# Performance work log

Hardware: AMD Instinct MI355X
Metric: run time of the kernel (lower is better)

## Reference

```python
import jax, jax.numpy as jnp
import numpy as np

C = 256

def setup_inputs() -> dict:
    key = jax.random.key(0)
    k1, k2, k3, k4, k5 = jax.random.split(key, 5)
    x = jax.random.normal(k1, (4, C, 64, 64), dtype=jnp.float32)
    # conv1x1 weights stored as (out, in) matrices
    w_qkv = jax.random.normal(k2, (3 * C, C), dtype=jnp.float32) * (1.0 / np.sqrt(C))
    b_qkv = jax.random.normal(k3, (3 * C,), dtype=jnp.float32) * 0.01
    w_out = jax.random.normal(k4, (C, C), dtype=jnp.float32) * (1.0 / np.sqrt(C))
    b_out = jax.random.normal(k5, (C,), dtype=jnp.float32) * 0.01
    return {"x": x, "w_qkv": w_qkv, "b_qkv": b_qkv, "w_out": w_out, "b_out": b_out}

def reference(x, w_qkv, b_qkv, w_out, b_out):
    b, c, h, w = x.shape
    # norm = Identity. conv1x1 == channel matmul
    qkv = jnp.einsum('bchw,oc->bohw', x, w_qkv) + b_qkv[None, :, None, None]
    q, k, v = jnp.split(qkv, 3, axis=1)  # each (b, c, h, w)
    q = q.reshape(b, c, h * w).transpose(0, 2, 1)  # (b, hw, c)
    k = k.reshape(b, c, h * w)                      # (b, c, hw)
    v = v.reshape(b, c, h * w).transpose(0, 2, 1)  # (b, hw, c)
    scores = jnp.einsum('bnc,bcm->bnm', q, k) * (c ** -0.5)  # (b, hw, hw)
    attn = jax.nn.softmax(scores, axis=-1)
    out = jnp.einsum('bnm,bmc->bnc', attn, v)  # (b, hw, c)
    out = out.transpose(0, 2, 1).reshape(b, c, h, w)
    out = jnp.einsum('bchw,oc->bohw', out, w_out) + b_out[None, :, None, None]
    return out + x
```

## Files before the change

kernel.cpp:

```cpp
#include <hip/hip_runtime.h>
#include <hip/hip_bf16.h>
#include <hip/hip_fp16.h>
#include <math.h>

typedef short s16x8 __attribute__((ext_vector_type(8)));
typedef float f32x4 __attribute__((ext_vector_type(4)));
typedef float f32x16 __attribute__((ext_vector_type(16)));
typedef unsigned short u16x4 __attribute__((ext_vector_type(4)));
typedef unsigned int u32x4 __attribute__((ext_vector_type(4)));

#define CCH 256
#define SEQ 4096
#define NB 4
#define KVB 64

static __device__ __forceinline__ unsigned short f2bf(float f) {
  union { float f; unsigned int u; } v; v.f = f;
  unsigned int u = v.u;
  unsigned int r = u + 0x7FFFu + ((u >> 16) & 1u);
  return (unsigned short)(r >> 16);
}

static __device__ __forceinline__ void gl16(const void* g, void* l) {
  __builtin_amdgcn_global_load_lds(
      (const __attribute__((address_space(1))) void*)g,
      (__attribute__((address_space(3))) void*)l, 16, 0, 0);
}

static __device__ __forceinline__ unsigned int cvt_pk_bf16(float lo, float hi) {
  unsigned int w;
  asm("v_cvt_pk_bf16_f32 %0, %1, %2" : "=v"(w) : "v"(lo), "v"(hi));
  return w;
}

__global__ __launch_bounds__(256) void prep(
    const float* __restrict__ wqkv, const float* __restrict__ wout,
    unsigned short* __restrict__ wqkb, unsigned short* __restrict__ wob)
{
  int bid = blockIdx.x;
  int tid = threadIdx.x;
  const float* src; unsigned short* dst; int i;
  if (bid < 192) { src = wqkv; dst = wqkb; i = bid * 256 + tid; }
  else           { src = wout; dst = wob;  i = (bid - 192) * 256 + tid; }
  float4 v = ((const float4*)src)[i];
  u16x4 r;
  r.x = f2bf(v.x); r.y = f2bf(v.y); r.z = f2bf(v.z); r.w = f2bf(v.w);
  ((u16x4*)dst)[i] = r;
}

__global__ __launch_bounds__(512) void qkv_proj(
    const float* __restrict__ x, const unsigned short* __restrict__ wqkb,
    const float* __restrict__ bias,
    unsigned short* __restrict__ qb, unsigned short* __restrict__ kb,
    unsigned short* __restrict__ vb)
{
  __shared__ __align__(16) unsigned short T[32][256];
  int b = blockIdx.y, st = blockIdx.x;
  int tid = threadIdx.x, w = tid >> 6, l = tid & 63, l15 = l & 15, lg = l >> 4;
  int sbase = st * 32;
  int s7 = l15 & 7;

  #pragma unroll
  for (int i = 0; i < 4; i++) {
    int idx = i * 512 + tid;
    int sc = idx & 7, ch = idx >> 3;
    float4 v = *(const float4*)&x[((size_t)b * CCH + ch) * SEQ + sbase + sc * 4];
    #pragma unroll
    for (int j = 0; j < 4; j++) {
      int s = sc * 4 + j;
      int csw = (((ch >> 3) ^ (s & 7)) << 3) | (ch & 7);
      float fv = (j == 0) ? v.x : (j == 1) ? v.y : (j == 2) ? v.z : v.w;
      T[s][csw] = f2bf(fv);
    }
  }
  __syncthreads();

  if (w < 4) {
    int sloc = (w & 1) * 16;
    int row0 = sbase + sloc;
    int osel = w >> 1;
    s16x8 af[8];
    #pragma unroll
    for (int t = 0; t < 8; t++)
      af[t] = *(const s16x8*)&T[sloc + l15][(((t * 4 + lg) ^ s7)) * 8];

    unsigned short* dst = osel ? kb : qb;
    #pragma unroll
    for (int ot = 0; ot < 16; ot++) {
      int orow = osel * 256 + ot * 16;
      f32x4 acc = (f32x4){0.f, 0.f, 0.f, 0.f};
      #pragma unroll
      for (int t = 0; t < 8; t++) {
        s16x8 wf = *(const s16x8*)&wqkb[(size_t)(orow + l15) * CCH + t * 32 + lg * 8];
        acc = __builtin_amdgcn_mfma_f32_16x16x32_bf16(af[t], wf, acc, 0, 0, 0);
      }
      float bi = bias[orow + l15];
      int ch = ot * 16 + l15;
      #pragma unroll
      for (int r = 0; r < 4; r++) {
        int srow = row0 + lg * 4 + r;
        dst[((size_t)b * SEQ + srow) * CCH + ch] = f2bf(acc[r] + bi);
      }
    }
  } else {
    int obase = (w - 4) * 64;
    f32x4 acc[4][2];
    #pragma unroll
    for (int i = 0; i < 4; i++)
      #pragma unroll
      for (int j = 0; j < 2; j++) acc[i][j] = (f32x4){0.f, 0.f, 0.f, 0.f};

    #pragma unroll
    for (int kt = 0; kt < 8; kt++) {
      s16x8 afr[4], bfr[2];
      #pragma unroll
      for (int ot = 0; ot < 4; ot++)
        afr[ot] = *(const s16x8*)&wqkb[(size_t)(512 + obase + ot * 16 + l15) * CCH + kt * 32 + lg * 8];
      #pragma unroll
      for (int sj = 0; sj < 2; sj++)
        bfr[sj] = *(const s16x8*)&T[sj * 16 + l15][(((kt * 4 + lg) ^ s7)) * 8];
      #pragma unroll
      for (int ot = 0; ot < 4; ot++)
        #pragma unroll
        for (int sj = 0; sj < 2; sj++)
          acc[ot][sj] = __builtin_amdgcn_mfma_f32_16x16x32_bf16(afr[ot], bfr[sj], acc[ot][sj], 0, 0, 0);
    }

    #pragma unroll
    for (int ot = 0; ot < 4; ot++) {
      #pragma unroll
      for (int r = 0; r < 4; r++) {
        int o = obase + ot * 16 + lg * 4 + r;
        float bi = bias[512 + o];
        #pragma unroll
        for (int sj = 0; sj < 2; sj++) {
          int s = sbase + sj * 16 + l15;
          vb[((size_t)b * CCH + o) * SEQ + s] = f2bf(acc[ot][sj][r] + bi);
        }
      }
    }
  }
}

template<int NSPLIT_>
__global__ __launch_bounds__(512, 2) void attn_kernel(
    const unsigned short* __restrict__ qb,
    const unsigned short* __restrict__ kb,
    const unsigned short* __restrict__ vb,
    __half* __restrict__ pacc, float* __restrict__ llp)
{
  constexpr int KVLEN_ = SEQ / NSPLIT_;
  constexpr int NT_ = KVLEN_ / KVB;
  __shared__ __align__(16) unsigned short Ks[2][KVB * CCH];
  __shared__ __align__(16) unsigned short Vs[2][CCH * KVB];

  int b = blockIdx.z, kvh = blockIdx.y, qt = blockIdx.x;
  int tid = threadIdx.x, w = tid >> 6, l = tid & 63;
  int l31 = l & 31, lh = l >> 5;
  int s7 = l31 & 7;

  int qrow0 = qt * 256 + w * 32;
  const unsigned short* qptr = qb + ((size_t)b * SEQ + qrow0 + l31) * CCH + lh * 8;
  s16x8 qf[16];
  #pragma unroll
  for (int t = 0; t < 16; t++) qf[t] = *(const s16x8*)(qptr + t * 16);

  f32x16 oacc[8];
  #pragma unroll
  for (int i = 0; i < 8; i++)
    #pragma unroll
    for (int j = 0; j < 16; j++) oacc[i][j] = 0.f;
  float ll = 0.f;

  int koff0 = (tid >> 5) * CCH + (((tid & 31) ^ ((tid >> 5) & 7)) * 8);
  int voff0 = (tid >> 3) * SEQ + (((tid & 7) ^ ((tid >> 3) & 7)) * 8);
  const unsigned short* kbb = kb + (size_t)b * SEQ * CCH + (size_t)kvh * KVLEN_ * CCH;
  const unsigned short* vbb = vb + (size_t)b * CCH * SEQ + kvh * KVLEN_;

  auto stage = [&](int bf_, int kv) {
    #pragma unroll
    for (int i = 0; i < 4; i++)
      gl16(kbb + (size_t)kv * KVB * CCH + koff0 + i * 16 * CCH, &Ks[bf_][(i * 512 + tid) * 8]);
    #pragma unroll
    for (int i = 0; i < 4; i++)
      gl16(vbb + kv * KVB + voff0 + (size_t)i * 64 * SEQ, &Vs[bf_][(i * 512 + tid) * 8]);
  };

  stage(0, 0);
  __syncthreads();

  int buf = 0;
  for (int kv = 0; kv < NT_; kv++) {
    if (kv + 1 < NT_) stage(buf ^ 1, kv + 1);

    #pragma unroll
    for (int h = 0; h < 2; h++) {
      f32x16 sacc;
      #pragma unroll
      for (int i = 0; i < 16; i++) sacc[i] = 0.f;
      __builtin_amdgcn_s_setprio(1);
      #pragma unroll
      for (int st = 0; st < 16; st++) {
        s16x8 kf = *(const s16x8*)&Ks[buf][(h * 32 + l31) * CCH + (((st * 2 + lh) ^ s7) * 8)];
        sacc = __builtin_amdgcn_mfma_f32_32x32x16_bf16(kf, qf[st], sacc, 0, 0, 0);
      }
      __builtin_amdgcn_s_setprio(0);

      unsigned int pw[8];
      #pragma unroll
      for (int r = 0; r < 8; r++) {
        float p0 = __builtin_amdgcn_exp2f(fmaf(sacc[2 * r],     0.09016844f, -11.5415602f));
        float p1 = __builtin_amdgcn_exp2f(fmaf(sacc[2 * r + 1], 0.09016844f, -11.5415602f));
        ll += p0 + p1;
        pw[r] = cvt_pk_bf16(p0, p1);
      }
      asm volatile("v_permlane32_swap_b32 %0, %1" : "+v"(pw[0]), "+v"(pw[2]));
      asm volatile("v_permlane32_swap_b32 %0, %1" : "+v"(pw[1]), "+v"(pw[3]));
      asm volatile("v_permlane32_swap_b32 %0, %1" : "+v"(pw[4]), "+v"(pw[6]));
      asm volatile("v_permlane32_swap_b32 %0, %1" : "+v"(pw[5]), "+v"(pw[7]));
      u32x4 pa0u = {pw[0], pw[1], pw[2], pw[3]};
      u32x4 pa1u = {pw[4], pw[5], pw[6], pw[7]};
      s16x8 pa0 = *(s16x8*)&pa0u;
      s16x8 pa1 = *(s16x8*)&pa1u;

      __builtin_amdgcn_s_setprio(1);
      #pragma unroll
      for (int dt = 0; dt < 8; dt++) {
        int base = (dt * 32 + l31) * KVB;
        s16x8 vf0 = *(const s16x8*)&Vs[buf][base + (((h * 4 + lh) ^ s7) * 8)];
        oacc[dt] = __builtin_amdgcn_mfma_f32_32x32x16_bf16(pa0, vf0, oacc[dt], 0, 0, 0);
        s16x8 vf1 = *(const s16x8*)&Vs[buf][base + (((h * 4 + 2 + lh) ^ s7) * 8)];
        oacc[dt] = __builtin_amdgcn_mfma_f32_32x32x16_bf16(pa1, vf1, oacc[dt], 0, 0, 0);
      }
      __builtin_amdgcn_s_setprio(0);
    }

    __syncthreads();
    buf ^= 1;
  }

  ll += __shfl_xor(ll, 32);
  size_t pbase = (size_t)(b * NSPLIT_ + kvh) * SEQ;
  if (lh == 0) llp[pbase + qrow0 + l31] = ll;
  __half* pb_ = pacc + (pbase + qrow0) * CCH + l31;
  #pragma unroll
  for (int rg = 0; rg < 4; rg++)
    #pragma unroll
    for (int j = 0; j < 4; j++) {
      int qr = j + 8 * rg + 4 * lh;
      #pragma unroll
      for (int dt = 0; dt < 8; dt++)
        pb_[(size_t)qr * CCH + dt * 32] = __float2half(oacc[dt][rg * 4 + j]);
    }
}

template<int NS>
__global__ __launch_bounds__(256) void out_proj(
    const __half* __restrict__ pacc, const float* __restrict__ llp,
    const unsigned short* __restrict__ wb,
    const float* __restrict__ bias, const float* __restrict__ x,
    float* __restrict__ out)
{
  int b = blockIdx.y, st = blockIdx.x;
  int tid = threadIdx.x, w = tid >> 6, l = tid & 63, l15 = l & 15, lg = l >> 4;
  int sbase = st * 32, obase = w * 64;

  float inv[2];
  #pragma unroll
  for (int sj = 0; sj < 2; sj++) {
    int s = sbase + sj * 16 + l15;
    float den = 0.f;
    #pragma unroll
    for (int k = 0; k < NS; k++) den += llp[(size_t)(b * NS + k) * SEQ + s];
    inv[sj] = 1.f / den;
  }

  f32x4 acc[4][2];
  #pragma unroll
  for (int i = 0; i < 4; i++)
    #pragma unroll
    for (int j = 0; j < 2; j++) acc[i][j] = (f32x4){0.f, 0.f, 0.f, 0.f};

  #pragma unroll
  for (int kt = 0; kt < 8; kt++) {
    s16x8 af[4], bfr[2];
    #pragma unroll
    for (int ot = 0; ot < 4; ot++)
      af[ot] = *(const s16x8*)&wb[(obase + ot * 16 + l15) * CCH + kt * 32 + lg * 8];
    #pragma unroll
    for (int sj = 0; sj < 2; sj++) {
      int s = sbase + sj * 16 + l15;
      float facc[8] = {0.f, 0.f, 0.f, 0.f, 0.f, 0.f, 0.f, 0.f};
      #pragma unroll
      for (int k = 0; k < NS; k++) {
        const __half* p = pacc + ((size_t)(b * NS + k) * SEQ + s) * CCH + kt * 32 + lg * 8;
        u16x4 h0 = *(const u16x4*)(p);
        u16x4 h1 = *(const u16x4*)(p + 4);
        #pragma unroll
        for (int j = 0; j < 4; j++) {
          facc[j]     += __half2float(*(const __half*)&((const unsigned short*)&h0)[j]);
          facc[4 + j] += __half2float(*(const __half*)&((const unsigned short*)&h1)[j]);
        }
      }
      unsigned short tmp[8];
      #pragma unroll
      for (int j = 0; j < 4; j++) {
        tmp[j]     = f2bf(facc[j] * inv[sj]);
        tmp[4 + j] = f2bf(facc[4 + j] * inv[sj]);
      }
      bfr[sj] = *(s16x8*)tmp;
    }
    #pragma unroll
    for (int ot = 0; ot < 4; ot++)
      #pragma unroll
      for (int sj = 0; sj < 2; sj++)
        acc[ot][sj] = __builtin_amdgcn_mfma_f32_16x16x32_bf16(af[ot], bfr[sj], acc[ot][sj], 0, 0, 0);
  }

  #pragma unroll
  for (int ot = 0; ot < 4; ot++) {
    #pragma unroll
    for (int r = 0; r < 4; r++) {
      int o = obase + ot * 16 + lg * 4 + r;
      float bi = bias[o];
      #pragma unroll
      for (int sj = 0; sj < 2; sj++) {
        int s = sbase + sj * 16 + l15;
        size_t idx = ((size_t)b * CCH + o) * SEQ + s;
        out[idx] = acc[ot][sj][r] + bi + x[idx];
      }
    }
  }
}

extern "C" void kernel_launch(void* const* d_in, const int* in_sizes, int n_in,
                              void* d_out, int out_size, void* d_ws, size_t ws_size,
                              hipStream_t stream) {
  const float* x     = (const float*)d_in[0];
  const float* w_qkv = (const float*)d_in[1];
  const float* b_qkv = (const float*)d_in[2];
  const float* w_out = (const float*)d_in[3];
  const float* b_out = (const float*)d_in[4];
  float* out = (float*)d_out;

  char* ws = (char*)d_ws;
  unsigned short* qbp  = (unsigned short*)(ws);
  unsigned short* kbp  = (unsigned short*)(ws + ((size_t)8 << 20));
  unsigned short* vbp  = (unsigned short*)(ws + ((size_t)16 << 20));
  unsigned short* wqkb = (unsigned short*)(ws + ((size_t)24 << 20));
  unsigned short* wob  = (unsigned short*)(ws + ((size_t)24 << 20) + (512u << 10));
  float*          llp  = (float*)(ws + ((size_t)25 << 20));
  __half*         pacc = (__half*)(ws + ((size_t)26 << 20));

  prep<<<dim3(256), 256, 0, stream>>>(w_qkv, w_out, wqkb, wob);
  qkv_proj<<<dim3(128, NB), 512, 0, stream>>>(x, wqkb, b_qkv, qbp, kbp, vbp);

  bool split4 = ws_size >= ((size_t)60 << 20);
  if (split4) {
    attn_kernel<4><<<dim3(16, 4, NB), 512, 0, stream>>>(qbp, kbp, vbp, pacc, llp);
    out_proj<4><<<dim3(128, NB), 256, 0, stream>>>(pacc, llp, wob, b_out, x, out);
  } else {
    attn_kernel<2><<<dim3(16, 2, NB), 512, 0, stream>>>(qbp, kbp, vbp, pacc, llp);
    out_proj<2><<<dim3(128, NB), 256, 0, stream>>>(pacc, llp, wob, b_out, x, out);
  }
}
```

Before: 150.0 us.

## Interleave second-half QK^T MFMAs with first-half PV MFMAs in attention loop

Restructures the per-KV-tile loop so the QK^T MFMAs for the second 32-row half are issued interleaved with the PV MFMAs of the first half. The goal is to overlap the softmax exp/permute latency with matrix work instead of running score, exp and PV strictly in sequence. The output-projection kernel also merges two 8-byte fp16 loads into one 16-byte load. It moves the 1/l normalization out of the per-element bf16 conversion into the final epilogue, which slightly changes rounding since unnormalized sums are converted to bf16.

```diff
diff --git a/kernel.cpp b/kernel.cpp
--- a/kernel.cpp
+++ b/kernel.cpp
@@ -7,6 +7,7 @@
 typedef float f32x4 __attribute__((ext_vector_type(4)));
 typedef float f32x16 __attribute__((ext_vector_type(16)));
 typedef unsigned short u16x4 __attribute__((ext_vector_type(4)));
+typedef unsigned short u16x8 __attribute__((ext_vector_type(8)));
 typedef unsigned int u32x4 __attribute__((ext_vector_type(4)));
 
 #define CCH 256
@@ -193,47 +194,82 @@
   for (int kv = 0; kv < NT_; kv++) {
     if (kv + 1 < NT_) stage(buf ^ 1, kv + 1);
 
-    #pragma unroll
-    for (int h = 0; h < 2; h++) {
-      f32x16 sacc;
-      #pragma unroll
-      for (int i = 0; i < 16; i++) sacc[i] = 0.f;
-      __builtin_amdgcn_s_setprio(1);
-      #pragma unroll
-      for (int st = 0; st < 16; st++) {
-        s16x8 kf = *(const s16x8*)&Ks[buf][(h * 32 + l31) * CCH + (((st * 2 + lh) ^ s7) * 8)];
-        sacc = __builtin_amdgcn_mfma_f32_32x32x16_bf16(kf, qf[st], sacc, 0, 0, 0);
-      }
-      __builtin_amdgcn_s_setprio(0);
-
-      unsigned int pw[8];
-      #pragma unroll
-      for (int r = 0; r < 8; r++) {
-        float p0 = __builtin_amdgcn_exp2f(fmaf(sacc[2 * r],     0.09016844f, -11.5415602f));
-        float p1 = __builtin_amdgcn_exp2f(fmaf(sacc[2 * r + 1], 0.09016844f, -11.5415602f));
-        ll += p0 + p1;
-        pw[r] = cvt_pk_bf16(p0, p1);
-      }
-      asm volatile("v_permlane32_swap_b32 %0, %1" : "+v"(pw[0]), "+v"(pw[2]));
-      asm volatile("v_permlane32_swap_b32 %0, %1" : "+v"(pw[1]), "+v"(pw[3]));
-      asm volatile("v_permlane32_swap_b32 %0, %1" : "+v"(pw[4]), "+v"(pw[6]));
-      asm volatile("v_permlane32_swap_b32 %0, %1" : "+v"(pw[5]), "+v"(pw[7]));
-      u32x4 pa0u = {pw[0], pw[1], pw[2], pw[3]};
-      u32x4 pa1u = {pw[4], pw[5], pw[6], pw[7]};
-      s16x8 pa0 = *(s16x8*)&pa0u;
-      s16x8 pa1 = *(s16x8*)&pa1u;
-
-      __builtin_amdgcn_s_setprio(1);
-      #pragma unroll
-      for (int dt = 0; dt < 8; dt++) {
-        int base = (dt * 32 + l31) * KVB;
-        s16x8 vf0 = *(const s16x8*)&Vs[buf][base + (((h * 4 + lh) ^ s7) * 8)];
-        oacc[dt] = __builtin_amdgcn_mfma_f32_32x32x16_bf16(pa0, vf0, oacc[dt], 0, 0, 0);
-        s16x8 vf1 = *(const s16x8*)&Vs[buf][base + (((h * 4 + 2 + lh) ^ s7) * 8)];
-        oacc[dt] = __builtin_amdgcn_mfma_f32_32x32x16_bf16(pa1, vf1, oacc[dt], 0, 0, 0);
-      }
-      __builtin_amdgcn_s_setprio(0);
-    }
+    const unsigned short* Kb = &Ks[buf][0];
+    const unsigned short* Vb = &Vs[buf][0];
+
+    f32x16 sacc0;
+    #pragma unroll
+    for (int i = 0; i < 16; i++) sacc0[i] = 0.f;
+    __builtin_amdgcn_s_setprio(1);
+    #pragma unroll
+    for (int st = 0; st < 16; st++) {
+      s16x8 kf = *(const s16x8*)&Kb[l31 * CCH + (((st * 2 + lh) ^ s7) * 8)];
+      sacc0 = __builtin_amdgcn_mfma_f32_32x32x16_bf16(kf, qf[st], sacc0, 0, 0, 0);
+    }
+    __builtin_amdgcn_s_setprio(0);
+
+    unsigned int pw0[8];
+    #pragma unroll
+    for (int r = 0; r < 8; r++) {
+      float p0 = __builtin_amdgcn_exp2f(fmaf(sacc0[2 * r],     0.09016844f, -11.5415602f));
+      float p1 = __builtin_amdgcn_exp2f(fmaf(sacc0[2 * r + 1], 0.09016844f, -11.5415602f));
+      ll += p0 + p1;
+      pw0[r] = cvt_pk_bf16(p0, p1);
+    }
+    asm volatile("v_permlane32_swap_b32 %0, %1" : "+v"(pw0[0]), "+v"(pw0[2]));
+    asm volatile("v_permlane32_swap_b32 %0, %1" : "+v"(pw0[1]), "+v"(pw0[3]));
+    asm volatile("v_permlane32_swap_b32 %0, %1" : "+v"(pw0[4]), "+v"(pw0[6]));
+    asm volatile("v_permlane32_swap_b32 %0, %1" : "+v"(pw0[5]), "+v"(pw0[7]));
+    u32x4 pa00u = {pw0[0], pw0[1], pw0[2], pw0[3]};
+    u32x4 pa01u = {pw0[4], pw0[5], pw0[6], pw0[7]};
+    s16x8 pa00 = *(s16x8*)&pa00u;
+    s16x8 pa01 = *(s16x8*)&pa01u;
+
+    f32x16 sacc1;
+    #pragma unroll
+    for (int i = 0; i < 16; i++) sacc1[i] = 0.f;
+    __builtin_amdgcn_s_setprio(1);
+    #pragma unroll
+    for (int i = 0; i < 8; i++) {
+      int base = (i * 32 + l31) * KVB;
+      s16x8 kfa = *(const s16x8*)&Kb[(32 + l31) * CCH + (((4 * i + lh) ^ s7) * 8)];
+      sacc1 = __builtin_amdgcn_mfma_f32_32x32x16_bf16(kfa, qf[2 * i], sacc1, 0, 0, 0);
+      s16x8 vf0 = *(const s16x8*)&Vb[base + ((lh ^ s7) * 8)];
+      oacc[i] = __builtin_amdgcn_mfma_f32_32x32x16_bf16(pa00, vf0, oacc[i], 0, 0, 0);
+      s16x8 kfb = *(const s16x8*)&Kb[(32 + l31) * CCH + (((4 * i + 2 + lh) ^ s7) * 8)];
+      sacc1 = __builtin_amdgcn_mfma_f32_32x32x16_bf16(kfb, qf[2 * i + 1], sacc1, 0, 0, 0);
+      s16x8 vf1 = *(const s16x8*)&Vb[base + (((2 + lh) ^ s7) * 8)];
+      oacc[i] = __builtin_amdgcn_mfma_f32_32x32x16_bf16(pa01, vf1, oacc[i], 0, 0, 0);
+    }
+    __builtin_amdgcn_s_setprio(0);
+
+    unsigned int pw1[8];
+    #pragma unroll
+    for (int r = 0; r < 8; r++) {
+      float p0 = __builtin_amdgcn_exp2f(fmaf(sacc1[2 * r],     0.09016844f, -11.5415602f));
+      float p1 = __builtin_amdgcn_exp2f(fmaf(sacc1[2 * r + 1], 0.09016844f, -11.5415602f));
+      ll += p0 + p1;
+      pw1[r] = cvt_pk_bf16(p0, p1);
+    }
+    asm volatile("v_permlane32_swap_b32 %0, %1" : "+v"(pw1[0]), "+v"(pw1[2]));
+    asm volatile("v_permlane32_swap_b32 %0, %1" : "+v"(pw1[1]), "+v"(pw1[3]));
+    asm volatile("v_permlane32_swap_b32 %0, %1" : "+v"(pw1[4]), "+v"(pw1[6]));
+    asm volatile("v_permlane32_swap_b32 %0, %1" : "+v"(pw1[5]), "+v"(pw1[7]));
+    u32x4 pa10u = {pw1[0], pw1[1], pw1[2], pw1[3]};
+    u32x4 pa11u = {pw1[4], pw1[5], pw1[6], pw1[7]};
+    s16x8 pa10 = *(s16x8*)&pa10u;
+    s16x8 pa11 = *(s16x8*)&pa11u;
+
+    __builtin_amdgcn_s_setprio(1);
+    #pragma unroll
+    for (int dt = 0; dt < 8; dt++) {
+      int base = (dt * 32 + l31) * KVB;
+      s16x8 vf0 = *(const s16x8*)&Vb[base + (((4 + lh) ^ s7) * 8)];
+      oacc[dt] = __builtin_amdgcn_mfma_f32_32x32x16_bf16(pa10, vf0, oacc[dt], 0, 0, 0);
+      s16x8 vf1 = *(const s16x8*)&Vb[base + (((6 + lh) ^ s7) * 8)];
+      oacc[dt] = __builtin_amdgcn_mfma_f32_32x32x16_bf16(pa11, vf1, oacc[dt], 0, 0, 0);
+    }
+    __builtin_amdgcn_s_setprio(0);
 
     __syncthreads();
     buf ^= 1;
@@ -294,20 +330,14 @@
       #pragma unroll
       for (int k = 0; k < NS; k++) {
         const __half* p = pacc + ((size_t)(b * NS + k) * SEQ + s) * CCH + kt * 32 + lg * 8;
-        u16x4 h0 = *(const u16x4*)(p);
-        u16x4 h1 = *(const u16x4*)(p + 4);
+        u16x8 h8 = *(const u16x8*)(p);
         #pragma unroll
-        for (int j = 0; j < 4; j++) {
-          facc[j]     += __half2float(*(const __half*)&((const unsigned short*)&h0)[j]);
-          facc[4 + j] += __half2float(*(const __half*)&((const unsigned short*)&h1)[j]);
-        }
+        for (int j = 0; j < 8; j++)
+          facc[j] += __half2float(*(const __half*)&((const unsigned short*)&h8)[j]);
       }
       unsigned short tmp[8];
       #pragma unroll
-      for (int j = 0; j < 4; j++) {
-        tmp[j]     = f2bf(facc[j] * inv[sj]);
-        tmp[4 + j] = f2bf(facc[4 + j] * inv[sj]);
-      }
+      for (int j = 0; j < 8; j++) tmp[j] = f2bf(facc[j]);
       bfr[sj] = *(s16x8*)tmp;
     }
     #pragma unroll
@@ -327,7 +357,7 @@
       for (int sj = 0; sj < 2; sj++) {
         int s = sbase + sj * 16 + l15;
         size_t idx = ((size_t)b * CCH + o) * SEQ + s;
-        out[idx] = acc[ot][sj][r] + bi + x[idx];
+        out[idx] = acc[ot][sj][r] * inv[sj] + bi + x[idx];
       }
     }
   }
```

After: 155.9 us. 1.04x slower.
